# Kernel optimization log

Hardware: AMD Instinct MI355X
Metric: run time of the kernel (lower is better)

Reference implementation:

```python
import jax, jax.numpy as jnp
import numpy as np

D_MODEL = 1024
NUM_HEADS = 16


def setup_inputs() -> dict:
    key = jax.random.key(0)
    ks = jax.random.split(key, 6)
    B, N, L, C = 16, 1024, 120, D_MODEL
    s = 0.02
    return {
        "x": jax.random.normal(ks[0], (B, N, C), jnp.float32),
        "cond": jax.random.normal(ks[1], (B, L, C), jnp.float32),
        "mask": jax.random.randint(ks[2], (B, L), 0, 2, jnp.int32),
        "Wq": jax.random.normal(ks[3], (C, C), jnp.float32) * s,
        "bq": jnp.zeros((C,), jnp.float32),
        "Wkv": jax.random.normal(ks[4], (2 * C, C), jnp.float32) * s,
        "bkv": jnp.zeros((2 * C,), jnp.float32),
        "Wp": jax.random.normal(ks[5], (C, C), jnp.float32) * s,
        "bp": jnp.zeros((C,), jnp.float32),
    }


def reference(x, cond, mask, Wq, bq, Wkv, bkv, Wp, bp):
    B, N, C = x.shape
    H = NUM_HEADS
    Dh = C // H
    scale = Dh ** (-0.5)
    # q: (B,H,N,Dh)
    q = (x @ Wq.T + bq).reshape(B, N, H, Dh).transpose(0, 2, 1, 3)
    # kv: (2,B,H,L,Dh)
    L = cond.shape[1]
    kv = (cond @ Wkv.T + bkv).reshape(B, L, 2, H, Dh).transpose(2, 0, 3, 1, 4)
    k, v = kv[0], kv[1]
    # attention scores (B,H,N,L)
    attn = jnp.einsum("bhnd,bhld->bhnl", q, k) * scale
    attn = jnp.where(mask[:, None, None, :] == 0, -jnp.inf, attn)
    attn = jax.nn.softmax(attn, axis=-1)
    out = jnp.einsum("bhnl,bhld->bhnd", attn, v)  # (B,H,N,Dh)
    out = out.transpose(0, 2, 1, 3).reshape(B, N, C)
    return out @ Wp.T + bp
```

## Files before the change

kernel.cpp:

```cpp
#include <hip/hip_runtime.h>

typedef unsigned short u16;
typedef unsigned int u32;
typedef float f32x4 __attribute__((ext_vector_type(4)));
typedef __bf16 bf16x8 __attribute__((ext_vector_type(8)));
typedef u32 u32x4 __attribute__((ext_vector_type(4)));
typedef u16 u16x4 __attribute__((ext_vector_type(4)));

#define NB 16
#define NSEQ 1024
#define NL 120
#define NLP 128
#define NC 1024
#define NH 16
#define NDH 64

__device__ __forceinline__ u16 f2bf(float f) {
  u32 u = __float_as_uint(f);
  return (u16)((u + 0x7fffu + ((u >> 16) & 1u)) >> 16);
}

__device__ __forceinline__ void gld_lds16(const void* g, void* l) {
  __builtin_amdgcn_global_load_lds(
      (const __attribute__((address_space(1))) void*)g,
      (__attribute__((address_space(3))) void*)l, 16, 0, 0);
}

__global__ __launch_bounds__(256) void cast_f32_bf16(const float* __restrict__ src,
                                                     u16* __restrict__ dst) {
  size_t i = ((size_t)blockIdx.x * 256 + threadIdx.x) * 4;
  f32x4 v = *(const f32x4*)(src + i);
  u16x4 o;
  o.x = f2bf(v.x); o.y = f2bf(v.y); o.z = f2bf(v.z); o.w = f2bf(v.w);
  *(u16x4*)(dst + i) = o;
}

template <bool OUT_F32>
__global__ __launch_bounds__(256) void gemm_bt(
    const u16* __restrict__ A, const u16* __restrict__ Bt,
    const float* __restrict__ bias, void* __restrict__ Cout,
    int M, int Nn, int K) {
  __shared__ u16 As[128 * 32];
  __shared__ u16 Bs[128 * 32];
  const int nt = Nn >> 7;
  const int bm = (int)blockIdx.x / nt;
  const int bn = (int)blockIdx.x % nt;
  const int m0 = bm << 7, n0 = bn << 7;
  const int tid = threadIdx.x;
  const int w = tid >> 6, lane = tid & 63;
  const int wm = (w & 1) << 6, wn = (w >> 1) << 6;
  const int quad = lane >> 4, l15 = lane & 15;

  f32x4 acc[4][4];
#pragma unroll
  for (int i = 0; i < 4; ++i)
#pragma unroll
    for (int j = 0; j < 4; ++j) acc[i][j] = (f32x4){0.f, 0.f, 0.f, 0.f};

  const int r0 = tid >> 2;
  const int cb = (tid & 3) << 3;
  const u16* aP = A + (size_t)(m0 + r0) * K + cb;
  const u16* bP = Bt + (size_t)(n0 + r0) * K + cb;
  u16* asDst = &As[r0 * 32 + cb];
  u16* bsDst = &Bs[r0 * 32 + cb];

  for (int k0 = 0; k0 < K; k0 += 32) {
    __syncthreads();
    gld_lds16(aP + k0, asDst);
    gld_lds16(aP + (size_t)64 * K + k0, asDst + 64 * 32);
    gld_lds16(bP + k0, bsDst);
    gld_lds16(bP + (size_t)64 * K + k0, bsDst + 64 * 32);
    __syncthreads();

    bf16x8 af[4], bfr[4];
#pragma unroll
    for (int i = 0; i < 4; ++i)
      af[i] = *(const bf16x8*)&As[(wm + i * 16 + l15) * 32 + quad * 8];
#pragma unroll
    for (int j = 0; j < 4; ++j)
      bfr[j] = *(const bf16x8*)&Bs[(wn + j * 16 + l15) * 32 + quad * 8];
#pragma unroll
    for (int i = 0; i < 4; ++i)
#pragma unroll
      for (int j = 0; j < 4; ++j)
        acc[i][j] =
            __builtin_amdgcn_mfma_f32_16x16x32_bf16(af[i], bfr[j], acc[i][j], 0, 0, 0);
  }

#pragma unroll
  for (int j = 0; j < 4; ++j) {
    const int col = n0 + wn + j * 16 + l15;
    const float bv = bias[col];
#pragma unroll
    for (int i = 0; i < 4; ++i) {
      const int row = m0 + wm + i * 16 + quad * 4;
#pragma unroll
      for (int r = 0; r < 4; ++r) {
        const float v = acc[i][j][r] + bv;
        if (OUT_F32)
          ((float*)Cout)[(size_t)(row + r) * Nn + col] = v;
        else
          ((u16*)Cout)[(size_t)(row + r) * Nn + col] = f2bf(v);
      }
    }
  }
}

__global__ __launch_bounds__(256) void attn(
    const u16* __restrict__ Qb, const u16* __restrict__ KVb,
    const int* __restrict__ mask, u16* __restrict__ Ob) {
  __shared__ u16 Ks[NLP * NDH];
  __shared__ u16 Vt[NDH * NLP];
  __shared__ float mb[NLP];
  __shared__ u16 pb[4][16 * NLP];

  const int b = (int)blockIdx.x >> 4;
  const int h = (int)blockIdx.x & 15;
  const int tid = threadIdx.x;
  const int w = tid >> 6, lane = tid & 63;
  const int quad = lane >> 4, l15 = lane & 15;
  const u16* kvbase = KVb + (size_t)b * NL * 2 * NC;

  for (int i = tid; i < NLP * 8; i += 256) {
    const int l = i >> 3, c8 = (i & 7) * 8;
    u32x4 z = {0u, 0u, 0u, 0u};
    u32x4 v = (l < NL) ? *(const u32x4*)(kvbase + (size_t)l * 2 * NC + h * NDH + c8) : z;
    *(u32x4*)&Ks[l * NDH + c8] = v;
  }
  u16* vstage = &pb[0][0];
  for (int i = tid; i < NL * 8; i += 256) {
    const int l = i >> 3, c8 = (i & 7) * 8;
    *(u32x4*)&vstage[l * NDH + c8] =
        *(const u32x4*)(kvbase + (size_t)l * 2 * NC + NC + h * NDH + c8);
  }
  for (int i = tid; i < NLP; i += 256)
    mb[i] = (i < NL && mask[b * NL + i] != 0) ? 0.0f : -1e30f;
  __syncthreads();
  for (int i = tid; i < NDH * NLP; i += 256) {
    const int d = i >> 7, l = i & 127;
    Vt[d * NLP + l] = (l < NL) ? vstage[l * NDH + d] : (u16)0;
  }
  __syncthreads();

  const float scale = 0.125f;
  for (int it = 0; it < 16; ++it) {
    const int q0 = it * 64 + w * 16;
    const u16* qptr = Qb + (size_t)(b * NSEQ + q0 + l15) * NC + h * NDH + quad * 8;
    const bf16x8 a0 = *(const bf16x8*)qptr;
    const bf16x8 a1 = *(const bf16x8*)(qptr + 32);

    f32x4 s[8];
#pragma unroll
    for (int kt = 0; kt < 8; ++kt) {
      const u16* kb = &Ks[(kt * 16 + l15) * NDH + quad * 8];
      const bf16x8 b0 = *(const bf16x8*)kb;
      const bf16x8 b1 = *(const bf16x8*)(kb + 32);
      f32x4 t = {0.f, 0.f, 0.f, 0.f};
      t = __builtin_amdgcn_mfma_f32_16x16x32_bf16(a0, b0, t, 0, 0, 0);
      t = __builtin_amdgcn_mfma_f32_16x16x32_bf16(a1, b1, t, 0, 0, 0);
      s[kt] = t;
    }
#pragma unroll
    for (int kt = 0; kt < 8; ++kt) {
      const float mbv = mb[kt * 16 + l15];
#pragma unroll
      for (int r = 0; r < 4; ++r) s[kt][r] = s[kt][r] * scale + mbv;
    }
    float sum[4];
#pragma unroll
    for (int r = 0; r < 4; ++r) {
      float m = s[0][r];
#pragma unroll
      for (int kt = 1; kt < 8; ++kt) m = fmaxf(m, s[kt][r]);
      m = fmaxf(m, __shfl_xor(m, 1));
      m = fmaxf(m, __shfl_xor(m, 2));
      m = fmaxf(m, __shfl_xor(m, 4));
      m = fmaxf(m, __shfl_xor(m, 8));
      float su = 0.f;
#pragma unroll
      for (int kt = 0; kt < 8; ++kt) {
        s[kt][r] = __expf(s[kt][r] - m);
        su += s[kt][r];
      }
      su += __shfl_xor(su, 1);
      su += __shfl_xor(su, 2);
      su += __shfl_xor(su, 4);
      su += __shfl_xor(su, 8);
      sum[r] = su;
    }
#pragma unroll
    for (int r = 0; r < 4; ++r) {
      const float inv = 1.0f / sum[r];
#pragma unroll
      for (int kt = 0; kt < 8; ++kt)
        pb[w][(quad * 4 + r) * NLP + kt * 16 + l15] = f2bf(s[kt][r] * inv);
    }
#pragma unroll
    for (int ntl = 0; ntl < 4; ++ntl) {
      f32x4 o = {0.f, 0.f, 0.f, 0.f};
#pragma unroll
      for (int kt = 0; kt < 4; ++kt) {
        const bf16x8 pa = *(const bf16x8*)&pb[w][l15 * NLP + kt * 32 + quad * 8];
        const bf16x8 vb = *(const bf16x8*)&Vt[(ntl * 16 + l15) * NLP + kt * 32 + quad * 8];
        o = __builtin_amdgcn_mfma_f32_16x16x32_bf16(pa, vb, o, 0, 0, 0);
      }
#pragma unroll
      for (int r = 0; r < 4; ++r)
        Ob[(size_t)(b * NSEQ + q0 + quad * 4 + r) * NC + h * NDH + ntl * 16 + l15] =
            f2bf(o[r]);
    }
  }
}

extern "C" void kernel_launch(void* const* d_in, const int* in_sizes, int n_in,
                              void* d_out, int out_size, void* d_ws, size_t ws_size,
                              hipStream_t stream) {
  const float* x = (const float*)d_in[0];
  const float* cond = (const float*)d_in[1];
  const int* mask = (const int*)d_in[2];
  const float* Wq = (const float*)d_in[3];
  const float* bq = (const float*)d_in[4];
  const float* Wkv = (const float*)d_in[5];
  const float* bkv = (const float*)d_in[6];
  const float* Wp = (const float*)d_in[7];
  const float* bp = (const float*)d_in[8];

  char* ws = (char*)d_ws;
  u16* xb = (u16*)(ws + 0);
  u16* condb = (u16*)(ws + 33554432);
  u16* Wqb = (u16*)(ws + 37486592);
  u16* Wkvb = (u16*)(ws + 39583744);
  u16* Wpb = (u16*)(ws + 43778048);
  u16* Qb = (u16*)(ws + 45875200);
  u16* KVb = (u16*)(ws + 79429632);
  u16* Ob = xb;

  cast_f32_bf16<<<16384, 256, 0, stream>>>(x, xb);
  cast_f32_bf16<<<1920, 256, 0, stream>>>(cond, condb);
  cast_f32_bf16<<<1024, 256, 0, stream>>>(Wq, Wqb);
  cast_f32_bf16<<<2048, 256, 0, stream>>>(Wkv, Wkvb);
  cast_f32_bf16<<<1024, 256, 0, stream>>>(Wp, Wpb);

  gemm_bt<false><<<128 * 8, 256, 0, stream>>>(xb, Wqb, bq, Qb, 16384, 1024, 1024);
  gemm_bt<false><<<15 * 16, 256, 0, stream>>>(condb, Wkvb, bkv, KVb, 1920, 2048, 1024);
  attn<<<256, 256, 0, stream>>>(Qb, KVb, mask, Ob);
  gemm_bt<true><<<128 * 8, 256, 0, stream>>>(Ob, Wpb, bp, d_out, 16384, 1024, 1024);
}
```

Before: 340.4 us.

## Fuse casts into one launch, split attention over query chunks, reorder GEMM tiles

The five cast launches become one kernel that picks its source buffer from the block index, which cuts launch overhead. The attention grid grows from 256 to 1024 blocks, each handling a quarter of the queries, so more of the GPU's compute units are kept busy. The cost is that K/V staging and the transpose are repeated four times per (batch, head). The GEMM tile order is also switched so consecutive blocks walk along M with a shared N tile, which changes cache reuse of the weight tiles.

```diff
diff --git a/kernel.cpp b/kernel.cpp
--- a/kernel.cpp
+++ b/kernel.cpp
@@ -26,9 +26,21 @@
       (__attribute__((address_space(3))) void*)l, 16, 0, 0);
 }
 
-__global__ __launch_bounds__(256) void cast_f32_bf16(const float* __restrict__ src,
-                                                     u16* __restrict__ dst) {
-  size_t i = ((size_t)blockIdx.x * 256 + threadIdx.x) * 4;
+__global__ __launch_bounds__(256) void cast_all(
+    const float* __restrict__ x, u16* __restrict__ xb,
+    const float* __restrict__ cond, u16* __restrict__ condb,
+    const float* __restrict__ Wq, u16* __restrict__ Wqb,
+    const float* __restrict__ Wkv, u16* __restrict__ Wkvb,
+    const float* __restrict__ Wp, u16* __restrict__ Wpb) {
+  int bk = blockIdx.x;
+  const float* src;
+  u16* dst;
+  if (bk < 16384) { src = x; dst = xb; }
+  else if (bk < 18304) { src = cond; dst = condb; bk -= 16384; }
+  else if (bk < 19328) { src = Wq; dst = Wqb; bk -= 18304; }
+  else if (bk < 21376) { src = Wkv; dst = Wkvb; bk -= 19328; }
+  else { src = Wp; dst = Wpb; bk -= 21376; }
+  size_t i = ((size_t)bk * 256 + threadIdx.x) * 4;
   f32x4 v = *(const f32x4*)(src + i);
   u16x4 o;
   o.x = f2bf(v.x); o.y = f2bf(v.y); o.z = f2bf(v.z); o.w = f2bf(v.w);
@@ -42,9 +54,9 @@
     int M, int Nn, int K) {
   __shared__ u16 As[128 * 32];
   __shared__ u16 Bs[128 * 32];
-  const int nt = Nn >> 7;
-  const int bm = (int)blockIdx.x / nt;
-  const int bn = (int)blockIdx.x % nt;
+  const int mt = M >> 7;
+  const int bm = (int)blockIdx.x % mt;
+  const int bn = (int)blockIdx.x / mt;
   const int m0 = bm << 7, n0 = bn << 7;
   const int tid = threadIdx.x;
   const int w = tid >> 6, lane = tid & 63;
@@ -114,8 +126,9 @@
   __shared__ float mb[NLP];
   __shared__ u16 pb[4][16 * NLP];
 
-  const int b = (int)blockIdx.x >> 4;
-  const int h = (int)blockIdx.x & 15;
+  const int chunk = (int)blockIdx.x & 3;
+  const int h = ((int)blockIdx.x >> 2) & 15;
+  const int b = (int)blockIdx.x >> 6;
   const int tid = threadIdx.x;
   const int w = tid >> 6, lane = tid & 63;
   const int quad = lane >> 4, l15 = lane & 15;
@@ -143,8 +156,8 @@
   __syncthreads();
 
   const float scale = 0.125f;
-  for (int it = 0; it < 16; ++it) {
-    const int q0 = it * 64 + w * 16;
+  for (int it = 0; it < 4; ++it) {
+    const int q0 = chunk * 256 + it * 64 + w * 16;
     const u16* qptr = Qb + (size_t)(b * NSEQ + q0 + l15) * NC + h * NDH + quad * 8;
     const bf16x8 a0 = *(const bf16x8*)qptr;
     const bf16x8 a1 = *(const bf16x8*)(qptr + 32);
@@ -235,14 +248,10 @@
   u16* KVb = (u16*)(ws + 79429632);
   u16* Ob = xb;
 
-  cast_f32_bf16<<<16384, 256, 0, stream>>>(x, xb);
-  cast_f32_bf16<<<1920, 256, 0, stream>>>(cond, condb);
-  cast_f32_bf16<<<1024, 256, 0, stream>>>(Wq, Wqb);
-  cast_f32_bf16<<<2048, 256, 0, stream>>>(Wkv, Wkvb);
-  cast_f32_bf16<<<1024, 256, 0, stream>>>(Wp, Wpb);
+  cast_all<<<22400, 256, 0, stream>>>(x, xb, cond, condb, Wq, Wqb, Wkv, Wkvb, Wp, Wpb);
 
   gemm_bt<false><<<128 * 8, 256, 0, stream>>>(xb, Wqb, bq, Qb, 16384, 1024, 1024);
   gemm_bt<false><<<15 * 16, 256, 0, stream>>>(condb, Wkvb, bkv, KVb, 1920, 2048, 1024);
-  attn<<<256, 256, 0, stream>>>(Qb, KVb, mask, Ob);
+  attn<<<1024, 256, 0, stream>>>(Qb, KVb, mask, Ob);
   gemm_bt<true><<<128 * 8, 256, 0, stream>>>(Ob, Wpb, bp, d_out, 16384, 1024, 1024);
 }
```

Result: faster. 331.6 us (-2.6%).
